# Optimization experiments

Measured on AMD Instinct MI355X. Metric: run time of the kernel, lower is better.

Reference implementation:

```python
import jax, jax.numpy as jnp
import numpy as np

B, N, L, E = 8, 2000, 128, 2048  # batch, nodes, local_size+1, ff_hidden_dim
PENALTY = 10.0


def setup_inputs() -> dict:
    key = jax.random.key(0)
    ks = jax.random.split(key, 8)
    dist = jax.random.uniform(ks[0], (B, N, N), jnp.float32) + 1e-3  # positive distances
    theta = jax.random.normal(ks[1], (B, N, N), jnp.float32)
    ins_feature0 = jax.random.normal(ks[2], (B, N, 1), jnp.float32)
    ins_feature1 = jax.random.normal(ks[3], (B, N, 1), jnp.float32)
    d_in = 2 * L + 2
    W1 = jax.random.normal(ks[4], (d_in, E), jnp.float32) * 0.02
    b1 = jnp.zeros((E,), jnp.float32)
    W2 = jax.random.normal(ks[5], (E, L), jnp.float32) * 0.02
    b2 = jnp.zeros((L,), jnp.float32)
    return {"theta": theta, "dist": dist, "ins_feature0": ins_feature0,
            "ins_feature1": ins_feature1, "W1": W1, "b1": b1, "W2": W2, "b2": b2}


def reference(theta, dist, ins_feature0, ins_feature1, W1, b1, W2, b2):
    k = W2.shape[1]  # local_size (L)
    # smallest-k along last dim, sorted ascending (torch.topk largest=False)
    neg_vals, idx = jax.lax.top_k(-dist, k)          # [B,N,L]
    sorted_dist = -neg_vals
    sorted_dist = sorted_dist / jnp.max(sorted_dist, axis=-1, keepdims=True)
    sorted_theta = jnp.take_along_axis(theta, idx, axis=-1)  # [B,N,L]
    x_in = jnp.concatenate([sorted_dist, sorted_theta, ins_feature0, ins_feature1], axis=-1)  # [B,N,2L+2]
    edge_emb = x_in @ W1 + b1                        # [B,N,E] (no nonlinearity, as in source)
    out = edge_emb @ W2 + b2 - sorted_dist           # [B,N,L]
    b_, n_, _ = dist.shape
    bi = jnp.arange(b_)[:, None, None]
    ni = jnp.arange(n_)[None, :, None]
    out_mat = jnp.full(dist.shape, PENALTY, dist.dtype).at[bi, ni, idx].set(out)
    return out_mat
```

## Files before the change

### kernel.cpp

```cpp
#include <hip/hip_runtime.h>
#include <hip/hip_bf16.h>

#define BN 8
#define NN 2000
#define LL 128
#define EE 2048
#define DIN 258
#define KPAD 264
#define NROWS (BN*NN)
#define PENALTY_V 10.0f
#define NBINS 256
#define CANDCAP 256
#define T0 0.092f
#define SPLITK 16
#define ECHUNK (EE/SPLITK)
#define RPB 4
#define AWORDS 2392

__global__ __launch_bounds__(256) void kA1(const float* __restrict__ W1,
                                           const float* __restrict__ b1,
                                           const float* __restrict__ W2,
                                           float* __restrict__ part) {
    __shared__ float As2[8][64];
    const int t = threadIdx.x;
    const int j = t & 127;
    const int half = t >> 7;
    const int rg = blockIdx.x >> 4;
    const int ks = blockIdx.x & 15;
    const int k0 = rg * 8;
    const int ebase = ks * ECHUNK;
    float acc[4] = {0.f, 0.f, 0.f, 0.f};
    for (int ec = ebase; ec < ebase + ECHUNK; ec += 64) {
        #pragma unroll
        for (int q = 0; q < 2; ++q) {
            int linear = q * 256 + t;
            int r8 = linear >> 6;
            int e  = linear & 63;
            int k  = k0 + r8;
            float v;
            if (k < DIN)       v = W1[k * EE + ec + e];
            else if (k == DIN) v = b1[ec + e];
            else               v = 0.0f;
            As2[r8][e] = v;
        }
        __syncthreads();
        #pragma unroll 8
        for (int e = 0; e < 64; ++e) {
            float w = W2[(ec + e) * LL + j];
            #pragma unroll
            for (int rr = 0; rr < 4; ++rr)
                acc[rr] += As2[half * 4 + rr][e] * w;
        }
        __syncthreads();
    }
    #pragma unroll
    for (int rr = 0; rr < 4; ++rr) {
        int k = k0 + half * 4 + rr;
        part[(size_t)ks * (KPAD * LL) + k * LL + j] = acc[rr];
    }
}

__global__ __launch_bounds__(256) void kA2(const float* __restrict__ part,
                                           const float* __restrict__ b2,
                                           float* __restrict__ Wc,
                                           float* __restrict__ bc) {
    const int i = blockIdx.x * 256 + threadIdx.x;
    float s = 0.f;
    #pragma unroll
    for (int q = 0; q < SPLITK; ++q) s += part[(size_t)q * (KPAD * LL) + i];
    const int k = i >> 7;
    const int j = i & 127;
    if (k == DIN)      { bc[j] = s + b2[j]; Wc[i] = 0.f; }
    else if (k > DIN)  { Wc[i] = 0.f; }
    else               { Wc[i] = s; }
}

__global__ __launch_bounds__(256) void kF(const float* __restrict__ dist,
                                          const float* __restrict__ theta,
                                          const float* __restrict__ f0,
                                          const float* __restrict__ f1,
                                          const float* __restrict__ Wc,
                                          const float* __restrict__ bc,
                                          float* __restrict__ out) {
    __shared__ __align__(16) unsigned int arena[RPB][AWORDS];
    const int t = threadIdx.x;
    const int lane = t & 63;
    const int w = t >> 6;
    const int row = blockIdx.x * RPB + w;

    unsigned int* A = arena[w];
    unsigned int* hist = A;
    unsigned long long* cand = (unsigned long long*)(A + 256);
    float* xv = (float*)(A + 2000);
    int* oidx = (int*)(A + 2264);

    {
        uint4 z4 = {0u, 0u, 0u, 0u};
        *(uint4*)&hist[lane * 4] = z4;
        unsigned long long f1v = ~0ULL;
        #pragma unroll
        for (int q = 0; q < CANDCAP / 64; ++q) cand[lane + q * 64] = f1v;
    }

    unsigned int v[32];
    const int nv = (lane < 52) ? 32 : 28;
    {
        const uint4* drow4 = (const uint4*)(dist + (size_t)row * NN);
        #pragma unroll
        for (int q = 0; q < 8; ++q) {
            int qi = q * 64 + lane;
            if (qi < NN / 4) {
                uint4 a = drow4[qi];
                v[4 * q]     = a.x;
                v[4 * q + 1] = a.y;
                v[4 * q + 2] = a.z;
                v[4 * q + 3] = a.w;
            }
        }
    }

    float T = T0;
    unsigned int qm = 0u;
    #pragma unroll
    for (int k = 0; k < 32; ++k)
        if (k < nv && __uint_as_float(v[k]) <= T) qm |= (1u << k);
    int cnt = __builtin_popcount(qm);
    #pragma unroll
    for (int d = 1; d < 64; d <<= 1) cnt += __shfl_xor(cnt, d);

    if (cnt < LL || cnt > CANDCAP) {
        unsigned int lmax = 0u;
        #pragma unroll
        for (int k = 0; k < 32; ++k) if (k < nv) lmax = max(lmax, v[k]);
        #pragma unroll
        for (int d = 1; d < 64; d <<= 1) lmax = max(lmax, (unsigned int)__shfl_xor((int)lmax, d));
        float lo = 0.0f, hi = __uint_as_float(lmax);
        if (cnt < LL) lo = T; else hi = T;
        for (int it = 0; it < 32; ++it) {
            T = 0.5f * (lo + hi);
            unsigned int m = 0u;
            #pragma unroll
            for (int k = 0; k < 32; ++k)
                if (k < nv && __uint_as_float(v[k]) <= T) m |= (1u << k);
            int c = __builtin_popcount(m);
            #pragma unroll
            for (int d = 1; d < 64; d <<= 1) c += __shfl_xor(c, d);
            qm = m;
            if (c >= LL && c <= CANDCAP) break;
            if (c < LL) lo = T; else hi = T;
        }
    }
    const float scale2 = (float)(NBINS - 1) / T;

    #pragma unroll
    for (int k = 0; k < 32; ++k) {
        if ((qm >> k) & 1u) {
            float f = __uint_as_float(v[k]);
            int b = (int)(f * scale2);
            b = b > NBINS - 1 ? NBINS - 1 : b;
            atomicAdd(&hist[b], 1u);
        }
    }

    {
        uint4* h4 = (uint4*)&hist[lane * 4];
        uint4 a0 = *h4;
        unsigned int c[4] = {a0.x, a0.y, a0.z, a0.w};
        unsigned int loc[4], run = 0;
        #pragma unroll
        for (int k = 0; k < 4; ++k) { loc[k] = run; run += c[k]; }
        unsigned int inc = run;
        #pragma unroll
        for (int d = 1; d < 64; d <<= 1) {
            unsigned int o = (unsigned int)__shfl_up((int)inc, d);
            if (lane >= d) inc += o;
        }
        const unsigned int excl = inc - run;
        uint4 s0 = {excl + loc[0], excl + loc[1], excl + loc[2], excl + loc[3]};
        *h4 = s0;
    }

    #pragma unroll
    for (int k = 0; k < 32; ++k) {
        if ((qm >> k) & 1u) {
            unsigned int bits = v[k];
            float f = __uint_as_float(bits);
            int b = (int)(f * scale2);
            b = b > NBINS - 1 ? NBINS - 1 : b;
            unsigned int old = atomicAdd(&hist[b], 0x10000u);
            unsigned int slot = (old & 0xFFFFu) + (old >> 16);
            unsigned int idx = (unsigned int)((k >> 2) * 256 + lane * 4 + (k & 3));
            if (slot < (unsigned int)CANDCAP)
                cand[slot] = ((unsigned long long)bits << 32) | idx;
        }
    }

    {
        unsigned long long key_s[CANDCAP / 64];
        float th_s[CANDCAP / 64];
        #pragma unroll
        for (int s = 0; s < CANDCAP / 64; ++s) key_s[s] = cand[lane + s * 64];
        #pragma unroll
        for (int s = 0; s < CANDCAP / 64; ++s)
            if (key_s[s] != ~0ULL)
                th_s[s] = theta[(size_t)row * NN + (unsigned int)key_s[s]];
        #pragma unroll
        for (int s = 0; s < CANDCAP / 64; ++s) {
            unsigned long long key = key_s[s];
            if (key != ~0ULL) {
                unsigned int bits = (unsigned int)(key >> 32);
                unsigned int idx  = (unsigned int)key;
                float f = __uint_as_float(bits);
                int b = (int)(f * scale2);
                b = b > NBINS - 1 ? NBINS - 1 : b;
                unsigned int word = hist[b];
                unsigned int start = word & 0xFFFFu;
                unsigned int end = start + (word >> 16);
                if (end > (unsigned int)CANDCAP) end = (unsigned int)CANDCAP;
                unsigned int r = start;
                for (unsigned int j = start; j < end; ++j) r += (cand[j] < key);
                if (r < (unsigned int)LL) {
                    xv[r] = f;
                    xv[LL + r] = th_s[s];
                    oidx[r] = (int)idx;
                }
            }
        }
    }

    {
        const float rdm = 1.0f / xv[LL - 1];
        xv[lane] *= rdm;
        xv[lane + 64] *= rdm;
        if (lane == 0) {
            xv[256] = f0[row];
            xv[257] = f1[row];
            #pragma unroll
            for (int z = DIN; z < KPAD; ++z) xv[z] = 0.0f;
        }
    }

    __syncthreads();

    #pragma unroll
    for (int r = 0; r < RPB; ++r) {
        float* rb = (float*)arena[r];
        for (int i = t; i < NN; i += 256) rb[i] = PENALTY_V;
    }

    const int j = t & 127;
    const int rp = t >> 7;
    const float* x0 = (const float*)(arena[2 * rp] + 2000);
    const float* x1 = (const float*)(arena[2 * rp + 1] + 2000);
    float acc0 = bc[j] - x0[j];
    float acc1 = bc[j] - x1[j];
    #pragma unroll 2
    for (int k = 0; k < KPAD; k += 4) {
        float4 xa = *(const float4*)&x0[k];
        float4 xb = *(const float4*)&x1[k];
        float w0 = Wc[(k + 0) * LL + j];
        float w1 = Wc[(k + 1) * LL + j];
        float w2 = Wc[(k + 2) * LL + j];
        float w3 = Wc[(k + 3) * LL + j];
        acc0 += xa.x * w0; acc1 += xb.x * w0;
        acc0 += xa.y * w1; acc1 += xb.y * w1;
        acc0 += xa.z * w2; acc1 += xb.z * w2;
        acc0 += xa.w * w3; acc1 += xb.w * w3;
    }

    __syncthreads();

    {
        float* rb0 = (float*)arena[2 * rp];
        float* rb1 = (float*)arena[2 * rp + 1];
        const int* oi0 = (const int*)(arena[2 * rp] + 2264);
        const int* oi1 = (const int*)(arena[2 * rp + 1] + 2264);
        rb0[oi0[j]] = acc0;
        rb1[oi1[j]] = acc1;
    }

    __syncthreads();

    {
        float4* o4 = (float4*)(out + (size_t)blockIdx.x * RPB * NN);
        for (int i = t; i < RPB * (NN / 4); i += 256) {
            int r = i / (NN / 4);
            int q = i - r * (NN / 4);
            o4[i] = ((const float4*)arena[r])[q];
        }
    }
}

extern "C" void kernel_launch(void* const* d_in, const int* in_sizes, int n_in,
                              void* d_out, int out_size, void* d_ws, size_t ws_size,
                              hipStream_t stream) {
    const float* theta = (const float*)d_in[0];
    const float* dist  = (const float*)d_in[1];
    const float* f0    = (const float*)d_in[2];
    const float* f1    = (const float*)d_in[3];
    const float* W1    = (const float*)d_in[4];
    const float* b1    = (const float*)d_in[5];
    const float* W2    = (const float*)d_in[6];
    const float* b2    = (const float*)d_in[7];
    float* out = (float*)d_out;

    char* ws = (char*)d_ws;
    float* Wc   = (float*)ws;
    float* bc   = (float*)(ws + 135168);
    float* part = (float*)(ws + 135680);

    kA1<<<33 * SPLITK, 256, 0, stream>>>(W1, b1, W2, part);
    kA2<<<(KPAD * LL) / 256, 256, 0, stream>>>(part, b2, Wc, bc);
    kF<<<NROWS / RPB, 256, 0, stream>>>(dist, theta, f0, f1, Wc, bc, out);
}
```

Baseline: 122.5 us.

## Shrink LDS arena and stage scatter output in three chunks for occupancy

Cuts the per-wave shared-memory arena from a full 2000-float row buffer to a 768-float chunk, so the penalty-fill, scatter and write-out steps now run in three passes over column chunks with extra barriers. The scatter indices are loaded into registers before the passes. Launch bounds now request 8 blocks per SM. This lowers LDS use per block to raise occupancy and hide memory latency in the top-k phase, at the cost of more __syncthreads and some idle threads in the final partial chunk.

```diff
diff --git a/kernel.cpp b/kernel.cpp
--- a/kernel.cpp
+++ b/kernel.cpp
@@ -15,7 +15,8 @@
 #define SPLITK 16
 #define ECHUNK (EE/SPLITK)
 #define RPB 4
-#define AWORDS 2392
+#define CHUNK 768
+#define AWORDS 1160
 
 __global__ __launch_bounds__(256) void kA1(const float* __restrict__ W1,
                                            const float* __restrict__ b1,
@@ -75,13 +76,13 @@
     else               { Wc[i] = s; }
 }
 
-__global__ __launch_bounds__(256) void kF(const float* __restrict__ dist,
-                                          const float* __restrict__ theta,
-                                          const float* __restrict__ f0,
-                                          const float* __restrict__ f1,
-                                          const float* __restrict__ Wc,
-                                          const float* __restrict__ bc,
-                                          float* __restrict__ out) {
+__global__ __launch_bounds__(256, 8) void kF(const float* __restrict__ dist,
+                                             const float* __restrict__ theta,
+                                             const float* __restrict__ f0,
+                                             const float* __restrict__ f1,
+                                             const float* __restrict__ Wc,
+                                             const float* __restrict__ bc,
+                                             float* __restrict__ out) {
     __shared__ __align__(16) unsigned int arena[RPB][AWORDS];
     const int t = threadIdx.x;
     const int lane = t & 63;
@@ -91,8 +92,8 @@
     unsigned int* A = arena[w];
     unsigned int* hist = A;
     unsigned long long* cand = (unsigned long long*)(A + 256);
-    float* xv = (float*)(A + 2000);
-    int* oidx = (int*)(A + 2264);
+    float* xv = (float*)(A + 768);
+    int* oidx = (int*)(A + 1032);
 
     {
         uint4 z4 = {0u, 0u, 0u, 0u};
@@ -242,16 +243,10 @@
 
     __syncthreads();
 
-    #pragma unroll
-    for (int r = 0; r < RPB; ++r) {
-        float* rb = (float*)arena[r];
-        for (int i = t; i < NN; i += 256) rb[i] = PENALTY_V;
-    }
-
     const int j = t & 127;
     const int rp = t >> 7;
-    const float* x0 = (const float*)(arena[2 * rp] + 2000);
-    const float* x1 = (const float*)(arena[2 * rp + 1] + 2000);
+    const float* x0 = (const float*)(arena[2 * rp] + 768);
+    const float* x1 = (const float*)(arena[2 * rp + 1] + 768);
     float acc0 = bc[j] - x0[j];
     float acc1 = bc[j] - x1[j];
     #pragma unroll 2
@@ -267,27 +262,34 @@
         acc0 += xa.z * w2; acc1 += xb.z * w2;
         acc0 += xa.w * w3; acc1 += xb.w * w3;
     }
+    const int oi0 = ((const int*)(arena[2 * rp] + 1032))[j];
+    const int oi1 = ((const int*)(arena[2 * rp + 1] + 1032))[j];
 
     __syncthreads();
 
-    {
-        float* rb0 = (float*)arena[2 * rp];
-        float* rb1 = (float*)arena[2 * rp + 1];
-        const int* oi0 = (const int*)(arena[2 * rp] + 2264);
-        const int* oi1 = (const int*)(arena[2 * rp + 1] + 2264);
-        rb0[oi0[j]] = acc0;
-        rb1[oi1[j]] = acc1;
-    }
-
-    __syncthreads();
-
-    {
-        float4* o4 = (float4*)(out + (size_t)blockIdx.x * RPB * NN);
-        for (int i = t; i < RPB * (NN / 4); i += 256) {
-            int r = i / (NN / 4);
-            int q = i - r * (NN / 4);
-            o4[i] = ((const float4*)arena[r])[q];
-        }
+    const float4 pen4 = {PENALTY_V, PENALTY_V, PENALTY_V, PENALTY_V};
+    #pragma unroll
+    for (int pass = 0; pass < 3; ++pass) {
+        const int lo = pass * CHUNK;
+        const int sw = (pass < 2) ? CHUNK : (NN - 2 * CHUNK);
+        const int s4 = sw >> 2;
+        #pragma unroll
+        for (int r = 0; r < RPB; ++r)
+            if (t < s4) ((float4*)arena[r])[t] = pen4;
+        __syncthreads();
+        {
+            if (oi0 >= lo && oi0 < lo + sw) ((float*)arena[2 * rp])[oi0 - lo] = acc0;
+            if (oi1 >= lo && oi1 < lo + sw) ((float*)arena[2 * rp + 1])[oi1 - lo] = acc1;
+        }
+        __syncthreads();
+        #pragma unroll
+        for (int r = 0; r < RPB; ++r) {
+            if (t < s4) {
+                float4* o4 = (float4*)(out + ((size_t)blockIdx.x * RPB + r) * NN + lo);
+                o4[t] = ((const float4*)arena[r])[t];
+            }
+        }
+        __syncthreads();
     }
 }
 
```

New measurement: 149.0 us. +21.6%, slower.
